# Kernel optimization log

Hardware: AMD Instinct MI355X
Metric: run time of the kernel (lower is better)

The kernel has to match this reference:

```python
import jax, jax.numpy as jnp
import numpy as np

B, S, D, H = 4, 2048, 1024, 1024  # batch, seq, input_dim, hidden_dim

def setup_inputs() -> dict:
    key = jax.random.key(0)
    k1, k2, k3, k4, k5 = jax.random.split(key, 5)
    scale1 = 1.0 / np.sqrt(D)
    scale2 = 1.0 / np.sqrt(H)
    return {
        "x": jax.random.normal(k1, (B, S, D), dtype=jnp.float32),
        "W1": jax.random.uniform(k2, (D, 3 * H), jnp.float32, -scale1, scale1),
        "b1": jax.random.uniform(k3, (3 * H,), jnp.float32, -scale1, scale1),
        "W2": jax.random.uniform(k4, (H, H), jnp.float32, -scale2, scale2),
        "b2": jax.random.uniform(k5, (H,), jnp.float32, -scale2, scale2),
    }

def reference(x, W1, b1, W2, b2):
    qkv = jnp.einsum('bsd,dh->bsh', x, W1) + b1          # [B,S,3H]
    q, k, v = jnp.split(qkv, 3, axis=-1)                  # each [B,S,H]
    scale = (2.0 * D) ** -0.5                             # faithful: (input_dim*2)^-0.5
    scores = jnp.einsum('bse,bSe->bsS', q, k) * scale     # [B,S,S]
    att = jax.nn.softmax(scores, axis=-1)
    ctx = jnp.einsum('bsS,bSe->bse', att, v)              # [B,S,H]
    out = jnp.einsum('bsh,hk->bsk', ctx, W2) + b2
    return out
```

## Files before the change

### kernel.cpp

```cpp
#include <hip/hip_runtime.h>
#include <hip/hip_bf16.h>
#include <stdint.h>

#define B_  4
#define S_  2048
#define D_  1024
#define H_  1024
#define BS_ (B_*S_)
#define N3H (3*H_)

typedef __bf16 bf16x8 __attribute__((ext_vector_type(8)));
typedef float  f32x4  __attribute__((ext_vector_type(4)));
typedef unsigned short u16x8 __attribute__((ext_vector_type(8)));
typedef unsigned short u16x4 __attribute__((ext_vector_type(4)));

__device__ __forceinline__ unsigned short f2bf(float x) {
    unsigned u = __float_as_uint(x);
    return (unsigned short)((u + 0x7FFFu + ((u >> 16) & 1u)) >> 16);
}
__device__ __forceinline__ float bf2f(unsigned short h) {
    return __uint_as_float(((unsigned)h) << 16);
}

__device__ __forceinline__ void gload_lds16(const void* g, void* l) {
    __builtin_amdgcn_global_load_lds(
        (const __attribute__((address_space(1))) void*)g,
        (__attribute__((address_space(3))) void*)l, 16, 0, 0);
}

#define BAR __builtin_amdgcn_s_barrier()
#define DS_FENCE do { asm volatile("s_waitcnt lgkmcnt(0)" ::: "memory"); \
                      __builtin_amdgcn_sched_barrier(0); } while (0)

template<int EPI, int SWZ>
__global__ __launch_bounds__(256, 3) void gemm3b(
    const unsigned short* __restrict__ A,
    const unsigned short* __restrict__ Bm,
    int NXt, int NYt, int N, int K, int Kst,
    long long sAz, long long sBz, long long sOz,
    void* __restrict__ out0, void* __restrict__ out1, void* __restrict__ out2,
    const float* __restrict__ bias, float scale)
{
    __shared__ __align__(16) char lds[3 * 16384];

    const int bid = (int)blockIdx.x;
    int tile;
    if constexpr (SWZ) {
        const int nt_g = (int)gridDim.x;
        const int C = nt_g >> 3;
        const int c = bid >> 3;
        const int xcd = bid & 7;
        const int qq = c >> 2;
        const int txl = qq % NXt;
        const int rest = (c & 3) + 4 * (qq / NXt);
        tile = xcd * C + rest * NXt + txl;
    } else {
        tile = bid;
    }
    const int tx = tile % NXt;
    const int rest2 = tile / NXt;
    const int ty = rest2 % NYt;
    const int tz = rest2 / NYt;

    const unsigned short* Ab = A  + (long long)tz * sAz;
    const unsigned short* Bb = Bm + (long long)tz * sBz;
    const int rowBase = ty * 128;
    const int colBase = tx * 128;
    const int tid = threadIdx.x;
    const int w = tid >> 6, l = tid & 63;
    const int wr = w >> 1, wc = w & 1;
    const int fr = l & 15, fq = l >> 4;

    int sr[2], scl[2];
#pragma unroll
    for (int j = 0; j < 2; j++) {
        int o  = j * 4096 + tid * 16;
        int st = o >> 10;
        int wi = o & 1023;
        wi ^= ((wi >> 9) & 1) << 5;
        sr[j]  = st * 16 + (wi >> 6);
        scl[j] = (wi & 63) >> 1;
    }

    auto STAGE_A = [&](char* buf, int t) {
        const unsigned short* base = Ab + (long long)rowBase * Kst + t * 32;
#pragma unroll
        for (int j = 0; j < 2; j++)
            gload_lds16(base + (long long)sr[j] * Kst + scl[j],
                        buf + j * 4096 + w * 1024);
    };
    auto STAGE_B = [&](char* buf, int t) {
        const unsigned short* base = Bb + (long long)colBase * Kst + t * 32;
#pragma unroll
        for (int j = 0; j < 2; j++)
            gload_lds16(base + (long long)sr[j] * Kst + scl[j],
                        buf + 8192 + j * 4096 + w * 1024);
    };

    const int abase = (fr * 64 + fq * 16) ^ ((fr & 8) << 2);

    f32x4 acc[4][4];
#pragma unroll
    for (int m = 0; m < 4; m++)
#pragma unroll
        for (int n = 0; n < 4; n++) acc[m][n] = (f32x4){0.f, 0.f, 0.f, 0.f};

    const int NT = K >> 5;

    STAGE_A(lds, 0); STAGE_B(lds, 0);
    STAGE_A(lds + 16384, 1); STAGE_B(lds + 16384, 1);
    asm volatile("s_waitcnt vmcnt(4)" ::: "memory");
    BAR;
    __builtin_amdgcn_sched_barrier(0);

    bf16x8 af[4], bf[4];

    for (int t = 0; t < NT; ++t) {
        const char* bc = lds + (t % 3) * 16384;
        char* bs = lds + ((t + 2) % 3) * 16384;
        int ts = t + 2; if (ts >= NT) ts -= NT;

#pragma unroll
        for (int m = 0; m < 4; m++)
            af[m] = *(const bf16x8*)(bc + (wr * 4 + m) * 1024 + abase);
#pragma unroll
        for (int n = 0; n < 4; n++)
            bf[n] = *(const bf16x8*)(bc + 8192 + (wc * 4 + n) * 1024 + abase);
        STAGE_A(bs, ts); STAGE_B(bs, ts);
        BAR; DS_FENCE;
        __builtin_amdgcn_s_setprio(1);
#pragma unroll
        for (int m = 0; m < 4; m++)
#pragma unroll
            for (int n = 0; n < 4; n++)
                acc[m][n] = __builtin_amdgcn_mfma_f32_16x16x32_bf16(
                    af[m], bf[n], acc[m][n], 0, 0, 0);
        __builtin_amdgcn_s_setprio(0);
        asm volatile("s_waitcnt vmcnt(4)" ::: "memory");
        BAR;
        __builtin_amdgcn_sched_barrier(0);
    }

    asm volatile("s_waitcnt vmcnt(0) lgkmcnt(0)" ::: "memory");
    BAR;

    const int crow0 = rowBase + wr * 64 + fq * 4;
    const int ccol0 = colBase + wc * 64 + fr;

    if constexpr (EPI == 0) {
        const int seg = colBase >> 10;
        if (seg < 2) {
            unsigned short* dst = (unsigned short*)(seg == 0 ? out0 : out1);
#pragma unroll
            for (int n = 0; n < 4; n++) {
                const int col = ccol0 + n * 16;
                const float bv = bias[col];
                const int scn = col & 1023;
#pragma unroll
                for (int m = 0; m < 4; m++) {
                    const int r0 = crow0 + m * 16;
#pragma unroll
                    for (int j = 0; j < 4; j++)
                        dst[(long long)(r0 + j) * 1024 + scn] = f2bf(acc[m][n][j] + bv);
                }
            }
        } else {
            unsigned short (*T)[129] = (unsigned short(*)[129])lds;
            const int lr0 = wr * 64 + fq * 4;
            const int lc0 = wc * 64 + fr;
#pragma unroll
            for (int n = 0; n < 4; n++) {
                const int lc = lc0 + n * 16;
#pragma unroll
                for (int m = 0; m < 4; m++)
#pragma unroll
                    for (int j = 0; j < 4; j++)
                        T[lr0 + m * 16 + j][lc] = f2bf(acc[m][n][j]);
            }
            BAR;
            const int s_loc = tid & 127, hh = tid >> 7;
            const int b = rowBase >> 11;
            const int s_glob = (rowBase & 2047) + s_loc;
            unsigned short* ut =
                (unsigned short*)out2 + (long long)b * ((long long)S_ * H_);
            const int h0 = (colBase - 2048) + hh * 64;
#pragma unroll 8
            for (int h = 0; h < 64; ++h)
                ut[(long long)(h0 + h) * S_ + s_glob] = T[s_loc][hh * 64 + h];
        }
    } else if constexpr (EPI == 6) {
        float* dst = (float*)out0 + (long long)tz * sOz;
#pragma unroll
        for (int n = 0; n < 4; n++) {
            const int col = ccol0 + n * 16;
#pragma unroll
            for (int m = 0; m < 4; m++) {
                const int r0 = crow0 + m * 16;
#pragma unroll
                for (int j = 0; j < 4; j++)
                    dst[(long long)(r0 + j) * N + col] = acc[m][n][j];
            }
        }
        (void)scale; (void)bias;
    } else {
        float* dst = (float*)out0 + (long long)tz * sOz;
        const float* bu = (const float*)out1;
#pragma unroll
        for (int m = 0; m < 4; m++) {
            float linv[4];
#pragma unroll
            for (int j = 0; j < 4; j++)
                linv[j] = 1.0f / bias[tz * 2048 + crow0 + m * 16 + j];
#pragma unroll
            for (int n = 0; n < 4; n++) {
                const int col = ccol0 + n * 16;
                const float bvv = bu[col];
                const int r0 = crow0 + m * 16;
#pragma unroll
                for (int j = 0; j < 4; j++)
                    dst[(long long)(r0 + j) * N + col] = acc[m][n][j] * linv[j] + bvv;
            }
        }
        (void)scale;
    }
}

template<int EPI>
__global__ __launch_bounds__(512, 2) void gemm256(
    const unsigned short* __restrict__ A,
    const unsigned short* __restrict__ Bm,
    int NXt, int NYt, int N, int K,
    long long sAz, long long sBz, long long sOz,
    void* __restrict__ out0, void* __restrict__ out1, void* __restrict__ out2,
    const float* __restrict__ bias, float scale)
{
    __shared__ __align__(16) char lds[131072];

    const int nt_g = (int)gridDim.x;
    const int bid = (int)blockIdx.x;
    const int C = nt_g >> 3;
    const int c = bid >> 3;
    const int xcd = bid & 7;
    const int qq = c >> 2;
    const int txl = qq % NXt;
    const int rest = (c & 3) + 4 * (qq / NXt);
    const int tile = xcd * C + rest * NXt + txl;
    const int tx = tile % NXt;
    const int rest2 = tile / NXt;
    const int ty = rest2 % NYt;
    const int tz = rest2 / NYt;

    const unsigned short* Ab = A  + (long long)tz * sAz;
    const unsigned short* Bb = Bm + (long long)tz * sBz;
    const int rowBase = ty * 256;
    const int colBase = tx * 256;
    const int tid = threadIdx.x;
    const int w = tid >> 6, l = tid & 63;
    const int wr = w >> 2, wc = w & 3;
    const int fr = l & 15, fq = l >> 4;

    int sr[2], scl[2];
#pragma unroll
    for (int j = 0; j < 2; j++) {
        int o  = j * 8192 + tid * 16;
        int st = o >> 10;
        int wi = o & 1023;
        wi ^= ((wi >> 9) & 1) << 5;
        sr[j]  = (st >> 1) * 16 + (wi >> 6);
        scl[j] = (st & 1) * 32 + ((wi & 63) >> 1);
    }

    auto STAGE = [&](int buf, int which, int tile_) {
        const unsigned short* mat = (which < 2) ? Ab : Bb;
        const int rt0 = ((which < 2) ? rowBase : colBase) + (which & 1) * 128;
        char* dst = lds + buf * 65536 + (which >> 1) * 32768
                        + (which & 1) * 16384 + w * 1024;
        const int k0 = tile_ * 64;
#pragma unroll
        for (int j = 0; j < 2; j++) {
            const unsigned short* src =
                mat + (long long)(rt0 + sr[j]) * K + k0 + scl[j];
            gload_lds16(src, dst + j * 8192);
        }
    };

    const int abase = (fr * 64 + fq * 16) ^ ((fr & 8) << 2);
    const char* Ah[2] = { lds + wr * 16384, lds + 65536 + wr * 16384 };
    const char* Bh[2] = { lds + 32768 + (wc >> 1) * 16384,
                          lds + 98304 + (wc >> 1) * 16384 };
    const int bn0 = (wc & 1) * 8192;

#define LA(b, m, kk) (*(const bf16x8*)(Ah[b] + (m)*2048 + (kk)*1024 + abase))
#define LB(b, n, kk) (*(const bf16x8*)(Bh[b] + bn0 + (n)*2048 + (kk)*1024 + abase))
#define MFMA16(AF, BF, MOFF, NOFF) do { \
    __builtin_amdgcn_s_setprio(1); \
    _Pragma("unroll") for (int m_ = 0; m_ < 4; m_++) \
    _Pragma("unroll") for (int n_ = 0; n_ < 2; n_++) \
    _Pragma("unroll") for (int k_ = 0; k_ < 2; k_++) \
        acc[(MOFF)+m_][(NOFF)+n_] = __builtin_amdgcn_mfma_f32_16x16x32_bf16( \
            AF[m_][k_], BF[n_][k_], acc[(MOFF)+m_][(NOFF)+n_], 0, 0, 0); \
    __builtin_amdgcn_s_setprio(0); } while (0)

    f32x4 acc[8][4];
#pragma unroll
    for (int m = 0; m < 8; m++)
#pragma unroll
        for (int n = 0; n < 4; n++) acc[m][n] = (f32x4){0.f, 0.f, 0.f, 0.f};

    const int NT = K >> 6;

    STAGE(0, 0, 0); STAGE(0, 1, 0); STAGE(0, 2, 0); STAGE(0, 3, 0);
    STAGE(1, 0, 1); STAGE(1, 1, 1);
    asm volatile("s_waitcnt vmcnt(4)" ::: "memory");
    BAR;
    __builtin_amdgcn_sched_barrier(0);

    bf16x8 afA[4][2], afB[4][2], bfA[2][2], bfB[2][2];

    for (int i = 0; i < NT / 2; i++) {
        const int t1 = 2 * i + 1;
        int t2 = 2 * i + 2; if (t2 >= NT) t2 -= NT;
        int t3 = 2 * i + 3; if (t3 >= NT) t3 -= NT;

#pragma unroll
        for (int m = 0; m < 4; m++) { afA[m][0] = LA(0, m, 0); afA[m][1] = LA(0, m, 1); }
#pragma unroll
        for (int n = 0; n < 2; n++) { bfA[n][0] = LB(0, n, 0); bfA[n][1] = LB(0, n, 1); }
        STAGE(1, 2, t1);
        BAR; DS_FENCE;
        MFMA16(afA, bfA, 0, 0);
        BAR;
#pragma unroll
        for (int m = 0; m < 4; m++) { afB[m][0] = LA(0, 4 + m, 0); afB[m][1] = LA(0, 4 + m, 1); }
        STAGE(1, 3, t1);
        BAR; DS_FENCE;
        MFMA16(afB, bfA, 4, 0);
        BAR;
#pragma unroll
        for (int n = 0; n < 2; n++) { bfB[n][0] = LB(0, 2 + n, 0); bfB[n][1] = LB(0, 2 + n, 1); }
        STAGE(0, 0, t2);
        BAR; DS_FENCE;
        MFMA16(afA, bfB, 0, 2);
        BAR;
        STAGE(0, 1, t2);
        BAR;
        MFMA16(afB, bfB, 4, 2);
        asm volatile("s_waitcnt vmcnt(4)" ::: "memory");
        BAR;
        __builtin_amdgcn_sched_barrier(0);

#pragma unroll
        for (int m = 0; m < 4; m++) { afA[m][0] = LA(1, m, 0); afA[m][1] = LA(1, m, 1); }
#pragma unroll
        for (int n = 0; n < 2; n++) { bfA[n][0] = LB(1, n, 0); bfA[n][1] = LB(1, n, 1); }
        STAGE(0, 2, t2);
        BAR; DS_FENCE;
        MFMA16(afA, bfA, 0, 0);
        BAR;
#pragma unroll
        for (int m = 0; m < 4; m++) { afB[m][0] = LA(1, 4 + m, 0); afB[m][1] = LA(1, 4 + m, 1); }
        STAGE(0, 3, t2);
        BAR; DS_FENCE;
        MFMA16(afB, bfA, 4, 0);
        BAR;
#pragma unroll
        for (int n = 0; n < 2; n++) { bfB[n][0] = LB(1, 2 + n, 0); bfB[n][1] = LB(1, 2 + n, 1); }
        STAGE(1, 0, t3);
        BAR; DS_FENCE;
        MFMA16(afA, bfB, 0, 2);
        BAR;
        STAGE(1, 1, t3);
        BAR;
        MFMA16(afB, bfB, 4, 2);
        asm volatile("s_waitcnt vmcnt(4)" ::: "memory");
        BAR;
        __builtin_amdgcn_sched_barrier(0);
    }

    asm volatile("s_waitcnt vmcnt(0) lgkmcnt(0)" ::: "memory");

    const int crow0 = rowBase + wr * 128 + fq * 4;
    const int ccol0 = colBase + wc * 64 + fr;

    if constexpr (EPI == 2) {
        float* lsum = (float*)out1;
        unsigned short* dst = (unsigned short*)out0 + (long long)tz * sOz;
#pragma unroll
        for (int m = 0; m < 8; m++) {
#pragma unroll
            for (int j = 0; j < 4; j++) {
                const int row = crow0 + m * 16 + j;
                float rs = 0.f;
#pragma unroll
                for (int n = 0; n < 4; n++) {
                    const int col = ccol0 + n * 16;
                    const float p = __expf(acc[m][n][j] * scale);
                    const unsigned short us = f2bf(p);
                    dst[(long long)row * N + col] = us;
                    rs += bf2f(us);
                }
                rs += __shfl_xor(rs, 1); rs += __shfl_xor(rs, 2);
                rs += __shfl_xor(rs, 4); rs += __shfl_xor(rs, 8);
                if (fr == 0) atomicAdd(&lsum[tz * 2048 + row], rs);
            }
        }
    }
    (void)out2; (void)bias;
#undef LA
#undef LB
#undef MFMA16
}

__global__ __launch_bounds__(256) void conv_f32_bf16(
    const float* __restrict__ in, unsigned short* __restrict__ out, int n8)
{
    for (int i = blockIdx.x * blockDim.x + threadIdx.x; i < n8;
         i += gridDim.x * blockDim.x) {
        const float4 a = ((const float4*)in)[2 * i];
        const float4 b = ((const float4*)in)[2 * i + 1];
        u16x8 o;
        o[0] = f2bf(a.x); o[1] = f2bf(a.y); o[2] = f2bf(a.z); o[3] = f2bf(a.w);
        o[4] = f2bf(b.x); o[5] = f2bf(b.y); o[6] = f2bf(b.z); o[7] = f2bf(b.w);
        ((u16x8*)out)[i] = o;
    }
}

__global__ __launch_bounds__(256) void conv_w1v(
    const float* __restrict__ W1, unsigned short* __restrict__ w1v)
{
    const int i = blockIdx.x * 256 + threadIdx.x;
    const int j = i >> 7, hh = (i & 127) * 8;
    const float4 a = *(const float4*)&W1[(long long)j * 3072 + 2048 + hh];
    const float4 b = *(const float4*)&W1[(long long)j * 3072 + 2048 + hh + 4];
    u16x8 o;
    o[0] = f2bf(a.x); o[1] = f2bf(a.y); o[2] = f2bf(a.z); o[3] = f2bf(a.w);
    o[4] = f2bf(b.x); o[5] = f2bf(b.y); o[6] = f2bf(b.z); o[7] = f2bf(b.w);
    *(u16x8*)&w1v[(long long)j * 1024 + hh] = o;
}

__global__ __launch_bounds__(256) void wu_reduce(
    const float* __restrict__ part, unsigned short* __restrict__ dst)
{
    const int i = blockIdx.x * 256 + threadIdx.x;
    f32x4 s = *(const f32x4*)&part[(long long)i * 4];
#pragma unroll
    for (int c = 1; c < 4; c++) {
        const f32x4 p = *(const f32x4*)&part[(long long)c * 1048576 + (long long)i * 4];
        s[0] += p[0]; s[1] += p[1]; s[2] += p[2]; s[3] += p[3];
    }
    u16x4 o;
    o[0] = f2bf(s[0]); o[1] = f2bf(s[1]); o[2] = f2bf(s[2]); o[3] = f2bf(s[3]);
    *(u16x4*)&dst[(long long)i * 4] = o;
}

__global__ __launch_bounds__(256) void bias_bu2(
    const float* __restrict__ b1, const unsigned short* __restrict__ w2t,
    const float* __restrict__ b2, float* __restrict__ bu2)
{
    const int i = blockIdx.x;
    const int t = threadIdx.x;
    const u16x4 wv = *(const u16x4*)&w2t[(long long)i * 1024 + t * 4];
    const float4 bv = *(const float4*)&b1[2048 + t * 4];
    float s = bv.x * bf2f(wv[0]) + bv.y * bf2f(wv[1])
            + bv.z * bf2f(wv[2]) + bv.w * bf2f(wv[3]);
    for (int o = 32; o; o >>= 1) s += __shfl_xor(s, o);
    __shared__ float red[4];
    if ((t & 63) == 0) red[t >> 6] = s;
    __syncthreads();
    if (t == 0) bu2[i] = red[0] + red[1] + red[2] + red[3] + b2[i];
}

__global__ __launch_bounds__(256) void tconv_f32_bf16(
    const float* __restrict__ in, unsigned short* __restrict__ out,
    int rows, int cols)
{
    __shared__ float t[32][33];
    const int c0 = blockIdx.x * 32, r0 = blockIdx.y * 32;
    const int tx = threadIdx.x & 31, ty = threadIdx.x >> 5;
#pragma unroll
    for (int i = 0; i < 4; i++)
        t[ty + 8 * i][tx] = in[(long long)(r0 + ty + 8 * i) * cols + c0 + tx];
    __syncthreads();
#pragma unroll
    for (int i = 0; i < 4; i++)
        out[(long long)(c0 + ty + 8 * i) * rows + r0 + tx] = f2bf(t[tx][ty + 8 * i]);
}

extern "C" void kernel_launch(void* const* d_in, const int* in_sizes, int n_in,
                              void* d_out, int out_size, void* d_ws, size_t ws_size,
                              hipStream_t stream)
{
    (void)in_sizes; (void)n_in; (void)out_size; (void)ws_size;
    const float* x  = (const float*)d_in[0];
    const float* W1 = (const float*)d_in[1];
    const float* b1 = (const float*)d_in[2];
    const float* W2 = (const float*)d_in[3];
    const float* b2 = (const float*)d_in[4];
    float* out = (float*)d_out;

    char* ws = (char*)d_ws;
    size_t off = 0;
    auto alloc = [&](size_t bytes) {
        void* p = ws + off;
        off += (bytes + 255) & ~(size_t)255;
        return p;
    };
    unsigned short* xbf = (unsigned short*)alloc((size_t)BS_ * D_ * 2);
    unsigned short* w1t = (unsigned short*)alloc((size_t)N3H * D_ * 2);
    unsigned short* w2t = (unsigned short*)alloc((size_t)H_ * H_ * 2);
    unsigned short* w1v = (unsigned short*)alloc((size_t)D_ * H_ * 2);
    unsigned short* q   = (unsigned short*)alloc((size_t)BS_ * H_ * 2);
    unsigned short* k   = (unsigned short*)alloc((size_t)BS_ * H_ * 2);
    unsigned short* ut  = (unsigned short*)alloc((size_t)BS_ * H_ * 2);
    unsigned short* sc  = (unsigned short*)alloc((size_t)B_ * S_ * S_ * 2);
    float*          lsum = (float*)alloc((size_t)BS_ * 4);
    float*          bu2  = (float*)alloc((size_t)H_ * 4);
    float*          part = (float*)sc;

    const float scale = 0.022097086912079608f;

    hipMemsetAsync(lsum, 0, (size_t)BS_ * 4, stream);

    conv_f32_bf16<<<dim3(2048), dim3(256), 0, stream>>>(x, xbf, BS_ * D_ / 8);
    tconv_f32_bf16<<<dim3(64, 32), dim3(256), 0, stream>>>(W1, w1t, D_, N3H);
    tconv_f32_bf16<<<dim3(32, 32), dim3(256), 0, stream>>>(W2, w2t, H_, H_);
    conv_w1v<<<dim3(512), dim3(256), 0, stream>>>(W1, w1v);

    gemm3b<6, 0><<<dim3(256), dim3(256), 0, stream>>>(
        w2t, w1v, 8, 8, 1024, 256, 1024, 256LL, 256LL, (long long)H_ * H_,
        part, nullptr, nullptr, nullptr, 1.0f);
    wu_reduce<<<dim3(1024), dim3(256), 0, stream>>>(part, w1t + (size_t)2048 * 1024);

    bias_bu2<<<dim3(1024), dim3(256), 0, stream>>>(b1, w2t, b2, bu2);

    gemm3b<0, 1><<<dim3(1536), dim3(256), 0, stream>>>(
        xbf, w1t, 24, 64, N3H, D_, D_, 0LL, 0LL, 0LL, q, k, ut, b1, 1.0f);

    gemm256<2><<<dim3(256), dim3(512), 0, stream>>>(
        q, k, 8, 8, S_, H_, (long long)S_ * H_, (long long)S_ * H_,
        (long long)S_ * S_, sc, lsum, nullptr, nullptr, scale);

    gemm3b<5, 1><<<dim3(512), dim3(256), 0, stream>>>(
        sc, ut, 8, 16, H_, S_, S_, (long long)S_ * S_, (long long)H_ * S_,
        (long long)S_ * H_, out, bu2, nullptr, lsum, 1.0f);
}
```

Baseline: 190.0 us.

## Split PV GEMM along K onto 256-tile kernel with separate combine pass

The final attention-times-V GEMM moves from the 128-tile gemm3b kernel to the larger 256x256 gemm256 kernel. The K dimension is split into two halves so the grid still has 256 blocks. Each half writes fp32 partials, one into the reused q buffer and one into out. A new combine_pv kernel sums the halves, applies the 1/rowsum normalization and adds the bias. This trades better tile efficiency and occupancy in the GEMM for an extra launch and an extra fp32 read/write pass over the output.

```diff
diff --git a/kernel.cpp b/kernel.cpp
--- a/kernel.cpp
+++ b/kernel.cpp
@@ -188,7 +188,7 @@
             for (int h = 0; h < 64; ++h)
                 ut[(long long)(h0 + h) * S_ + s_glob] = T[s_loc][hh * 64 + h];
         }
-    } else if constexpr (EPI == 6) {
+    } else {
         float* dst = (float*)out0 + (long long)tz * sOz;
 #pragma unroll
         for (int n = 0; n < 4; n++) {
@@ -202,26 +202,6 @@
             }
         }
         (void)scale; (void)bias;
-    } else {
-        float* dst = (float*)out0 + (long long)tz * sOz;
-        const float* bu = (const float*)out1;
-#pragma unroll
-        for (int m = 0; m < 4; m++) {
-            float linv[4];
-#pragma unroll
-            for (int j = 0; j < 4; j++)
-                linv[j] = 1.0f / bias[tz * 2048 + crow0 + m * 16 + j];
-#pragma unroll
-            for (int n = 0; n < 4; n++) {
-                const int col = ccol0 + n * 16;
-                const float bvv = bu[col];
-                const int r0 = crow0 + m * 16;
-#pragma unroll
-                for (int j = 0; j < 4; j++)
-                    dst[(long long)(r0 + j) * N + col] = acc[m][n][j] * linv[j] + bvv;
-            }
-        }
-        (void)scale;
     }
 }
 
@@ -229,7 +209,7 @@
 __global__ __launch_bounds__(512, 2) void gemm256(
     const unsigned short* __restrict__ A,
     const unsigned short* __restrict__ Bm,
-    int NXt, int NYt, int N, int K,
+    int NXt, int NYt, int N, int K, int Kst,
     long long sAz, long long sBz, long long sOz,
     void* __restrict__ out0, void* __restrict__ out1, void* __restrict__ out2,
     const float* __restrict__ bias, float scale)
@@ -250,8 +230,14 @@
     const int ty = rest2 % NYt;
     const int tz = rest2 / NYt;
 
-    const unsigned short* Ab = A  + (long long)tz * sAz;
-    const unsigned short* Bb = Bm + (long long)tz * sBz;
+    long long aoz = (long long)tz * sAz;
+    long long boz = (long long)tz * sBz;
+    if constexpr (EPI == 7) {
+        aoz = (long long)(tz & 3) * sAz + (long long)(tz >> 2) * 1024;
+        boz = (long long)(tz & 3) * sBz + (long long)(tz >> 2) * 1024;
+    }
+    const unsigned short* Ab = A  + aoz;
+    const unsigned short* Bb = Bm + boz;
     const int rowBase = ty * 256;
     const int colBase = tx * 256;
     const int tid = threadIdx.x;
@@ -279,7 +265,7 @@
 #pragma unroll
         for (int j = 0; j < 2; j++) {
             const unsigned short* src =
-                mat + (long long)(rt0 + sr[j]) * K + k0 + scl[j];
+                mat + (long long)(rt0 + sr[j]) * Kst + k0 + scl[j];
             gload_lds16(src, dst + j * 8192);
         }
     };
@@ -404,11 +390,43 @@
                 if (fr == 0) atomicAdd(&lsum[tz * 2048 + row], rs);
             }
         }
+    } else if constexpr (EPI == 7) {
+        const int pvb = tz & 3, pvch = tz >> 2;
+        float* dst = (float*)(pvch ? out1 : out0)
+                   + (long long)pvb * ((long long)S_ * H_);
+#pragma unroll
+        for (int m = 0; m < 8; m++) {
+#pragma unroll
+            for (int n = 0; n < 4; n++) {
+                const int col = ccol0 + n * 16;
+                const int r0 = crow0 + m * 16;
+#pragma unroll
+                for (int j = 0; j < 4; j++)
+                    dst[(long long)(r0 + j) * N + col] = acc[m][n][j];
+            }
+        }
     }
     (void)out2; (void)bias;
 #undef LA
 #undef LB
 #undef MFMA16
+}
+
+__global__ __launch_bounds__(256) void combine_pv(
+    const float* __restrict__ p0, float* __restrict__ out,
+    const float* __restrict__ lsum, const float* __restrict__ bu2)
+{
+    const int i4 = blockIdx.x * 256 + threadIdx.x;
+    const int row = i4 >> 8;
+    const int col = (i4 & 255) * 4;
+    const float linv = 1.0f / lsum[row];
+    const f32x4 a = *(const f32x4*)&p0[(long long)i4 * 4];
+    const f32x4 b = *(const f32x4*)&out[(long long)i4 * 4];
+    const f32x4 bu = *(const f32x4*)&bu2[col];
+    f32x4 r;
+#pragma unroll
+    for (int e = 0; e < 4; e++) r[e] = (a[e] + b[e]) * linv + bu[e];
+    *(f32x4*)&out[(long long)i4 * 4] = r;
 }
 
 __global__ __launch_bounds__(256) void conv_f32_bf16(
@@ -516,6 +534,7 @@
     float*          lsum = (float*)alloc((size_t)BS_ * 4);
     float*          bu2  = (float*)alloc((size_t)H_ * 4);
     float*          part = (float*)sc;
+    float*          pvp0 = (float*)q;
 
     const float scale = 0.022097086912079608f;
 
@@ -537,10 +556,12 @@
         xbf, w1t, 24, 64, N3H, D_, D_, 0LL, 0LL, 0LL, q, k, ut, b1, 1.0f);
 
     gemm256<2><<<dim3(256), dim3(512), 0, stream>>>(
-        q, k, 8, 8, S_, H_, (long long)S_ * H_, (long long)S_ * H_,
+        q, k, 8, 8, S_, H_, H_, (long long)S_ * H_, (long long)S_ * H_,
         (long long)S_ * S_, sc, lsum, nullptr, nullptr, scale);
 
-    gemm3b<5, 1><<<dim3(512), dim3(256), 0, stream>>>(
-        sc, ut, 8, 16, H_, S_, S_, (long long)S_ * S_, (long long)H_ * S_,
-        (long long)S_ * H_, out, bu2, nullptr, lsum, 1.0f);
-}
+    gemm256<7><<<dim3(256), dim3(512), 0, stream>>>(
+        sc, ut, 4, 8, H_, 1024, S_, (long long)S_ * S_, (long long)H_ * S_,
+        0LL, pvp0, out, nullptr, nullptr, 1.0f);
+
+    combine_pv<<<dim3(8192), dim3(256), 0, stream>>>(pvp0, out, lsum, bu2);
+}
```

Measured after the change: 199.5 us. 5.0% more time.
